# Optimization experiments

Hardware: AMD Instinct MI355X
Metric: run time of the kernel (lower is better)

## Reference

```python
import jax, jax.numpy as jnp
import numpy as np

N, B, CIN = 2048, 16, 1
M = 4096
COUT = 64
R = 128


def setup_inputs() -> dict:
    key = jax.random.key(0)
    k1, k2, k3, k4, k5 = jax.random.split(key, 5)
    return {
        "context_in": jax.random.normal(k1, (N, B, CIN), dtype=jnp.float32),
        "context_out": jax.random.normal(k2, (N, B, COUT), dtype=jnp.float32),
        "target_in": jax.random.normal(k3, (M, B, CIN), dtype=jnp.float32),
        "lengthscale": jnp.ones((1,), dtype=jnp.float32),
        "W": jax.random.normal(k4, (R, COUT + 1), dtype=jnp.float32),
        "b": jax.random.normal(k5, (R,), dtype=jnp.float32),
    }


def reference(context_in, context_out, target_in, lengthscale, W, b):
    # context_in: (N,B,Cin), context_out: (N,B,Cout), target_in: (M,B,Cin)
    n, batch, _ = context_in.shape
    # density channel prepended -> (N,B,Cout+1)
    dens = jnp.ones((n, batch, 1), dtype=context_in.dtype)
    co = jnp.concatenate([dens, context_out], axis=-1)
    ci = jnp.transpose(context_in, (1, 0, 2))   # (B,N,Cin)
    ti = jnp.transpose(target_in, (1, 0, 2))    # (B,M,Cin)
    # squared pairwise distances (B,N,M)
    d2 = (jnp.sum(ci * ci, -1)[:, :, None]
          + jnp.sum(ti * ti, -1)[:, None, :]
          - 2.0 * jnp.einsum('bnd,bmd->bnm', ci, ti))
    d2 = jnp.maximum(d2, 0.0)
    # RBF kernel: exp(-0.5 * d2 / lengthscale^2)
    K = jnp.exp(-0.5 * d2 / (lengthscale[0] ** 2))  # (B,N,M)
    # weighted sum over context points: (B,M,Cout+1)
    out = jnp.einsum('nbc,bnm->bmc', co, K)
    # density normalization of non-density channels
    out = jnp.concatenate([out[..., :1], out[..., 1:] / (out[..., :1] + 1e-8)], axis=-1)
    # linear projection (Cout+1 -> R)
    out = out @ W.T + b
    return jnp.transpose(out, (1, 0, 2))  # (M,B,R)
```

## Files before the change

### kernel.cpp

```cpp
#include <hip/hip_runtime.h>
#include <hip/hip_bf16.h>


#define N_CTX 2048
#define BATCH 16
#define M_TGT 4096
#define COUT  64
#define RDIM  128
#define TN    64
#define NTILES (N_CTX / TN)

typedef __attribute__((ext_vector_type(8)))  short        bf16x8;
typedef __attribute__((ext_vector_type(4)))  unsigned int uint4v;
typedef __attribute__((ext_vector_type(16))) float        floatx16;

#if __has_builtin(__builtin_amdgcn_exp2f)
#define EXP2F __builtin_amdgcn_exp2f
#else
#define EXP2F exp2f
#endif

static __device__ __forceinline__ unsigned int pack_bf16(float lo, float hi) {
    __hip_bfloat162 h = __float22bfloat162_rn(make_float2(lo, hi));
    return *reinterpret_cast<unsigned int*>(&h);
}
static __device__ __forceinline__ unsigned short f2bf(float f) {
    __hip_bfloat16 h = __float2bfloat16(f);
    return *reinterpret_cast<unsigned short*>(&h);
}

__global__ __launch_bounds__(256)
void convdeepset_mfma(const float* __restrict__ ci, const float* __restrict__ co,
                      const float* __restrict__ ti, const float* __restrict__ ls,
                      const float* __restrict__ W,  const float* __restrict__ bias,
                      float* __restrict__ out)
{
    __shared__ unsigned short co_t[4096];
    __shared__ unsigned short wt[8192];
    __shared__ unsigned short vstage[4 * 2048];
    __shared__ float x_t[TN];
    __shared__ float w0l[RDIM];
    __shared__ float biasl[RDIM];

    const int tid  = threadIdx.x;
    const int lane = tid & 63;
    const int wv   = tid >> 6;
    const int g    = lane >> 5;
    const int l31  = lane & 31;
    const int b    = blockIdx.x >> 5;
    const int mt   = blockIdx.x & 31;

    for (int e = tid; e < 4096; e += 256) {
        const int ch  = e >> 9;
        const int rem = e & 511;
        const int r   = rem >> 2;
        const int tp  = (rem & 3) << 1;
        const float f0 = W[r * 65 + 1 + ch * 8 + tp];
        const float f1 = W[r * 65 + 2 + ch * 8 + tp];
        *reinterpret_cast<unsigned int*>(&wt[ch * 1024 + r * 8 + tp]) = pack_bf16(f0, f1);
    }
    if (tid < RDIM) { w0l[tid] = W[tid * 65]; biasl[tid] = bias[tid]; }

    const int m0    = mt * 128 + wv * 32;
    const float y   = ti[(size_t)(m0 + l31) * BATCH + b];
    const float lsv = ls[0];
    const float fc2 = (-0.5f / (lsv * lsv)) * 1.4426950408889634f;

    const int sc = tid & 63;
    const int sn = (tid >> 6) * 16;
    const float* cob = co + (size_t)b * COUT + sc;

    float pf[16];
#pragma unroll
    for (int q = 0; q < 8; ++q) {
        pf[2*q]   = cob[(size_t)(sn + 2*q)     * (BATCH * COUT)];
        pf[2*q+1] = cob[(size_t)(sn + 2*q + 1) * (BATCH * COUT)];
    }
    float xpf = (tid < TN) ? ci[(size_t)tid * BATCH + b] : 0.0f;

    floatx16 acc0, acc1;
#pragma unroll
    for (int i = 0; i < 16; ++i) { acc0[i] = 0.0f; acc1[i] = 0.0f; }
    float dens = 0.0f;

    for (int t = 0; t < NTILES; ++t) {
        __syncthreads();
#pragma unroll
        for (int q = 0; q < 8; ++q) {
            const int noff = sn + 2*q;
            *reinterpret_cast<unsigned int*>(&co_t[(noff >> 3) * 512 + sc * 8 + (noff & 7)])
                = pack_bf16(pf[2*q], pf[2*q+1]);
        }
        if (tid < TN) x_t[tid] = xpf;
        __syncthreads();
        if (t + 1 < NTILES) {
            const int n0n = (t + 1) * TN;
#pragma unroll
            for (int q = 0; q < 8; ++q) {
                pf[2*q]   = cob[(size_t)(n0n + sn + 2*q)     * (BATCH * COUT)];
                pf[2*q+1] = cob[(size_t)(n0n + sn + 2*q + 1) * (BATCH * COUT)];
            }
            if (tid < TN) xpf = ci[(size_t)(n0n + tid) * BATCH + b];
        }
#pragma unroll
        for (int s = 0; s < 4; ++s) {
            const float* xp = &x_t[s * 16 + g * 8];
            const float4 xa = *(const float4*)(xp);
            const float4 xb = *(const float4*)(xp + 4);
            const float xs[8] = {xa.x, xa.y, xa.z, xa.w, xb.x, xb.y, xb.z, xb.w};
            float kv[8];
#pragma unroll
            for (int j = 0; j < 8; ++j) {
                const float d = xs[j] - y;
                kv[j] = EXP2F(fc2 * d * d);
                dens += kv[j];
            }
            uint4v aw;
#pragma unroll
            for (int q = 0; q < 4; ++q) aw[q] = pack_bf16(kv[2*q], kv[2*q+1]);
            const bf16x8 av = __builtin_bit_cast(bf16x8, aw);
            const int ch = 2 * s + g;
            const bf16x8 b0 = *reinterpret_cast<const bf16x8*>(&co_t[ch * 512 + l31 * 8]);
            const bf16x8 b1 = *reinterpret_cast<const bf16x8*>(&co_t[ch * 512 + l31 * 8 + 256]);
            acc0 = __builtin_amdgcn_mfma_f32_32x32x16_bf16(av, b0, acc0, 0, 0, 0);
            acc1 = __builtin_amdgcn_mfma_f32_32x32x16_bf16(av, b1, acc1, 0, 0, 0);
        }
    }

    dens += __shfl_xor(dens, 32);

    float drow[16];
    unsigned short* vs = vstage + wv * 2048;
#pragma unroll
    for (int reg = 0; reg < 16; ++reg) {
        const int row = (reg & 3) + 8 * (reg >> 2) + 4 * g;
        const float dr = __shfl(dens, row);
        drow[reg] = dr;
        const float dinv = 1.0f / (dr + 1e-8f);
        const float v0 = acc0[reg] * dinv;
        const float v1 = acc1[reg] * dinv;
        const int c0 = l31, c1 = 32 + l31;
        vs[(c0 >> 3) * 256 + row * 8 + (c0 & 7)] = f2bf(v0);
        vs[(c1 >> 3) * 256 + row * 8 + (c1 & 7)] = f2bf(v1);
    }

    floatx16 pacc[4];
#pragma unroll
    for (int rt = 0; rt < 4; ++rt)
#pragma unroll
        for (int i = 0; i < 16; ++i) pacc[rt][i] = 0.0f;

#pragma unroll
    for (int s2 = 0; s2 < 4; ++s2) {
        const int ch = 2 * s2 + g;
        const bf16x8 avp = *reinterpret_cast<const bf16x8*>(&vs[ch * 256 + l31 * 8]);
#pragma unroll
        for (int rt = 0; rt < 4; ++rt) {
            const bf16x8 bvp = *reinterpret_cast<const bf16x8*>(&wt[ch * 1024 + (rt * 32 + l31) * 8]);
            pacc[rt] = __builtin_amdgcn_mfma_f32_32x32x16_bf16(avp, bvp, pacc[rt], 0, 0, 0);
        }
    }

#pragma unroll
    for (int rt = 0; rt < 4; ++rt) {
        const int r = rt * 32 + l31;
        const float w0v = w0l[r];
        const float bv  = biasl[r];
#pragma unroll
        for (int reg = 0; reg < 16; ++reg) {
            const int row = (reg & 3) + 8 * (reg >> 2) + 4 * g;
            const float val = pacc[rt][reg] + drow[reg] * w0v + bv;
            out[((size_t)(m0 + row) * BATCH + b) * RDIM + r] = val;
        }
    }
}

extern "C" void kernel_launch(void* const* d_in, const int* in_sizes, int n_in,
                              void* d_out, int out_size, void* d_ws, size_t ws_size,
                              hipStream_t stream) {
    const float* ci   = (const float*)d_in[0];
    const float* co   = (const float*)d_in[1];
    const float* ti   = (const float*)d_in[2];
    const float* ls   = (const float*)d_in[3];
    const float* W    = (const float*)d_in[4];
    const float* bias = (const float*)d_in[5];
    float* o = (float*)d_out;
    (void)in_sizes; (void)n_in; (void)out_size; (void)d_ws; (void)ws_size;

    const int grid = BATCH * (M_TGT / 128);
    convdeepset_mfma<<<grid, 256, 0, stream>>>(ci, co, ti, ls, W, bias, o);
}
```

Baseline: 134.0 us.

## Precompute bf16 MFMA-layout context and scaled inputs in a prep kernel

Adds a preprocessing kernel that converts context_out to bf16 in the exact MFMA B-operand layout, pre-scales context inputs by sqrt(0.5*log2e)/lengthscale, and packs W into workspace. The main kernel then streams B fragments straight from global memory with register double-buffering, with no per-tile LDS staging or __syncthreads. Blocks shrink to 128 threads with 64 targets each, doubling the grid. The cost is an extra launch and the global traffic of the prep pass, and each block still rereads the whole bf16 context for its batch from L2.

```diff
diff --git a/kernel.cpp b/kernel.cpp
--- a/kernel.cpp
+++ b/kernel.cpp
@@ -7,8 +7,12 @@
 #define M_TGT 4096
 #define COUT  64
 #define RDIM  128
-#define TN    64
-#define NTILES (N_CTX / TN)
+
+#define WS_CO_BYTES (N_CTX * BATCH * COUT * 2)
+#define WS_SX_OFF   WS_CO_BYTES
+#define WS_WT_OFF   (WS_SX_OFF + N_CTX * BATCH * 4)
+
+#define SSCALE 0.8493222f
 
 typedef __attribute__((ext_vector_type(8)))  short        bf16x8;
 typedef __attribute__((ext_vector_type(4)))  unsigned int uint4v;
@@ -30,120 +34,118 @@
 }
 
 __global__ __launch_bounds__(256)
-void convdeepset_mfma(const float* __restrict__ ci, const float* __restrict__ co,
-                      const float* __restrict__ ti, const float* __restrict__ ls,
+void convdeepset_prep(const float* __restrict__ ci, const float* __restrict__ co,
+                      const float* __restrict__ ls, const float* __restrict__ W,
+                      unsigned char* __restrict__ ws)
+{
+    unsigned short* cow = (unsigned short*)ws;
+    float*          sx  = (float*)(ws + WS_SX_OFF);
+    unsigned short* wt  = (unsigned short*)(ws + WS_WT_OFF);
+    const int blk = blockIdx.x, tid = threadIdx.x;
+
+    if (blk < 4096) {
+        const int f  = blk * 256 + tid;
+        const int c  = f & 63;
+        const int bb = (f >> 6) & 15;
+        const int n  = (f >> 10) * 2;
+        const float f0 = co[((size_t)n       * BATCH + bb) * COUT + c];
+        const float f1 = co[((size_t)(n + 1) * BATCH + bb) * COUT + c];
+        const int gch = n >> 3, e = n & 7;
+        *(unsigned int*)&cow[bb * 131072 + gch * 512 + c * 8 + e] = pack_bf16(f0, f1);
+    } else if (blk < 4224) {
+        const int f = (blk - 4096) * 256 + tid;
+        const int n = f & 2047, bb = f >> 11;
+        const float s = SSCALE / ls[0];
+        sx[bb * 2048 + n] = s * ci[(size_t)n * BATCH + bb];
+    } else {
+        for (int f = tid; f < 8192; f += 256) {
+            const int cp = f & 7, r = (f >> 3) & 127, ch = f >> 10;
+            wt[ch * 1024 + r * 8 + cp] = f2bf(W[r * 65 + 1 + ch * 8 + cp]);
+        }
+    }
+}
+
+__global__ __launch_bounds__(128)
+void convdeepset_main(const float* __restrict__ ti, const float* __restrict__ ls,
                       const float* __restrict__ W,  const float* __restrict__ bias,
-                      float* __restrict__ out)
+                      const unsigned char* __restrict__ ws, float* __restrict__ out)
 {
-    __shared__ unsigned short co_t[4096];
-    __shared__ unsigned short wt[8192];
-    __shared__ unsigned short vstage[4 * 2048];
-    __shared__ float x_t[TN];
-    __shared__ float w0l[RDIM];
-    __shared__ float biasl[RDIM];
+    __shared__ float sxt[N_CTX];
+    __shared__ unsigned short vstage[2][2048];
 
     const int tid  = threadIdx.x;
     const int lane = tid & 63;
     const int wv   = tid >> 6;
     const int g    = lane >> 5;
     const int l31  = lane & 31;
-    const int b    = blockIdx.x >> 5;
-    const int mt   = blockIdx.x & 31;
+    const int b    = blockIdx.x >> 6;
+    const int mt   = blockIdx.x & 63;
+    const int m0   = mt * 64 + wv * 32;
 
-    for (int e = tid; e < 4096; e += 256) {
-        const int ch  = e >> 9;
-        const int rem = e & 511;
-        const int r   = rem >> 2;
-        const int tp  = (rem & 3) << 1;
-        const float f0 = W[r * 65 + 1 + ch * 8 + tp];
-        const float f1 = W[r * 65 + 2 + ch * 8 + tp];
-        *reinterpret_cast<unsigned int*>(&wt[ch * 1024 + r * 8 + tp]) = pack_bf16(f0, f1);
-    }
-    if (tid < RDIM) { w0l[tid] = W[tid * 65]; biasl[tid] = bias[tid]; }
+    const float4* sxg = (const float4*)(ws + WS_SX_OFF) + b * (N_CTX / 4);
+    float4* sxt4 = (float4*)sxt;
+#pragma unroll
+    for (int q = 0; q < 4; ++q) sxt4[q * 128 + tid] = sxg[q * 128 + tid];
 
-    const int m0    = mt * 128 + wv * 32;
-    const float y   = ti[(size_t)(m0 + l31) * BATCH + b];
-    const float lsv = ls[0];
-    const float fc2 = (-0.5f / (lsv * lsv)) * 1.4426950408889634f;
+    const float s  = SSCALE / ls[0];
+    const float sy = s * ti[(size_t)(m0 + l31) * BATCH + b];
+    __syncthreads();
 
-    const int sc = tid & 63;
-    const int sn = (tid >> 6) * 16;
-    const float* cob = co + (size_t)b * COUT + sc;
-
-    float pf[16];
-#pragma unroll
-    for (int q = 0; q < 8; ++q) {
-        pf[2*q]   = cob[(size_t)(sn + 2*q)     * (BATCH * COUT)];
-        pf[2*q+1] = cob[(size_t)(sn + 2*q + 1) * (BATCH * COUT)];
-    }
-    float xpf = (tid < TN) ? ci[(size_t)tid * BATCH + b] : 0.0f;
+    const unsigned short* cow = (const unsigned short*)ws
+                              + (size_t)b * 131072 + g * 512 + l31 * 8;
 
     floatx16 acc0, acc1;
 #pragma unroll
     for (int i = 0; i < 16; ++i) { acc0[i] = 0.0f; acc1[i] = 0.0f; }
     float dens = 0.0f;
 
-    for (int t = 0; t < NTILES; ++t) {
-        __syncthreads();
+    bf16x8 cb0 = *(const bf16x8*)(cow);
+    bf16x8 cb1 = *(const bf16x8*)(cow + 256);
+    float4 xa  = *(const float4*)&sxt[g * 8];
+    float4 xb  = *(const float4*)&sxt[g * 8 + 4];
+
+    for (int ks = 0; ks < 128; ++ks) {
+        bf16x8 nb0 = cb0, nb1 = cb1; float4 nxa = xa, nxb = xb;
+        if (ks < 127) {
+            const unsigned short* p = cow + (ks + 1) * 1024;
+            nb0 = *(const bf16x8*)(p);
+            nb1 = *(const bf16x8*)(p + 256);
+            nxa = *(const float4*)&sxt[(ks + 1) * 16 + g * 8];
+            nxb = *(const float4*)&sxt[(ks + 1) * 16 + g * 8 + 4];
+        }
+        const float xs[8] = {xa.x, xa.y, xa.z, xa.w, xb.x, xb.y, xb.z, xb.w};
+        float kv[8];
 #pragma unroll
-        for (int q = 0; q < 8; ++q) {
-            const int noff = sn + 2*q;
-            *reinterpret_cast<unsigned int*>(&co_t[(noff >> 3) * 512 + sc * 8 + (noff & 7)])
-                = pack_bf16(pf[2*q], pf[2*q+1]);
+        for (int j = 0; j < 8; ++j) {
+            const float t = xs[j] - sy;
+            kv[j] = EXP2F(-(t * t));
+            dens += kv[j];
         }
-        if (tid < TN) x_t[tid] = xpf;
-        __syncthreads();
-        if (t + 1 < NTILES) {
-            const int n0n = (t + 1) * TN;
+        uint4v aw;
 #pragma unroll
-            for (int q = 0; q < 8; ++q) {
-                pf[2*q]   = cob[(size_t)(n0n + sn + 2*q)     * (BATCH * COUT)];
-                pf[2*q+1] = cob[(size_t)(n0n + sn + 2*q + 1) * (BATCH * COUT)];
-            }
-            if (tid < TN) xpf = ci[(size_t)(n0n + tid) * BATCH + b];
-        }
-#pragma unroll
-        for (int s = 0; s < 4; ++s) {
-            const float* xp = &x_t[s * 16 + g * 8];
-            const float4 xa = *(const float4*)(xp);
-            const float4 xb = *(const float4*)(xp + 4);
-            const float xs[8] = {xa.x, xa.y, xa.z, xa.w, xb.x, xb.y, xb.z, xb.w};
-            float kv[8];
-#pragma unroll
-            for (int j = 0; j < 8; ++j) {
-                const float d = xs[j] - y;
-                kv[j] = EXP2F(fc2 * d * d);
-                dens += kv[j];
-            }
-            uint4v aw;
-#pragma unroll
-            for (int q = 0; q < 4; ++q) aw[q] = pack_bf16(kv[2*q], kv[2*q+1]);
-            const bf16x8 av = __builtin_bit_cast(bf16x8, aw);
-            const int ch = 2 * s + g;
-            const bf16x8 b0 = *reinterpret_cast<const bf16x8*>(&co_t[ch * 512 + l31 * 8]);
-            const bf16x8 b1 = *reinterpret_cast<const bf16x8*>(&co_t[ch * 512 + l31 * 8 + 256]);
-            acc0 = __builtin_amdgcn_mfma_f32_32x32x16_bf16(av, b0, acc0, 0, 0, 0);
-            acc1 = __builtin_amdgcn_mfma_f32_32x32x16_bf16(av, b1, acc1, 0, 0, 0);
-        }
+        for (int q = 0; q < 4; ++q) aw[q] = pack_bf16(kv[2 * q], kv[2 * q + 1]);
+        const bf16x8 av = __builtin_bit_cast(bf16x8, aw);
+        acc0 = __builtin_amdgcn_mfma_f32_32x32x16_bf16(av, cb0, acc0, 0, 0, 0);
+        acc1 = __builtin_amdgcn_mfma_f32_32x32x16_bf16(av, cb1, acc1, 0, 0, 0);
+        cb0 = nb0; cb1 = nb1; xa = nxa; xb = nxb;
     }
 
     dens += __shfl_xor(dens, 32);
 
     float drow[16];
-    unsigned short* vs = vstage + wv * 2048;
+    unsigned short* vs = vstage[wv];
 #pragma unroll
     for (int reg = 0; reg < 16; ++reg) {
         const int row = (reg & 3) + 8 * (reg >> 2) + 4 * g;
         const float dr = __shfl(dens, row);
         drow[reg] = dr;
         const float dinv = 1.0f / (dr + 1e-8f);
-        const float v0 = acc0[reg] * dinv;
-        const float v1 = acc1[reg] * dinv;
         const int c0 = l31, c1 = 32 + l31;
-        vs[(c0 >> 3) * 256 + row * 8 + (c0 & 7)] = f2bf(v0);
-        vs[(c1 >> 3) * 256 + row * 8 + (c1 & 7)] = f2bf(v1);
+        vs[(c0 >> 3) * 256 + row * 8 + (c0 & 7)] = f2bf(acc0[reg] * dinv);
+        vs[(c1 >> 3) * 256 + row * 8 + (c1 & 7)] = f2bf(acc1[reg] * dinv);
     }
 
+    const unsigned short* wtg = (const unsigned short*)(ws + WS_WT_OFF);
     floatx16 pacc[4];
 #pragma unroll
     for (int rt = 0; rt < 4; ++rt)
@@ -153,10 +155,10 @@
 #pragma unroll
     for (int s2 = 0; s2 < 4; ++s2) {
         const int ch = 2 * s2 + g;
-        const bf16x8 avp = *reinterpret_cast<const bf16x8*>(&vs[ch * 256 + l31 * 8]);
+        const bf16x8 avp = *(const bf16x8*)&vs[ch * 256 + l31 * 8];
 #pragma unroll
         for (int rt = 0; rt < 4; ++rt) {
-            const bf16x8 bvp = *reinterpret_cast<const bf16x8*>(&wt[ch * 1024 + (rt * 32 + l31) * 8]);
+            const bf16x8 bvp = *(const bf16x8*)&wtg[ch * 1024 + (rt * 32 + l31) * 8];
             pacc[rt] = __builtin_amdgcn_mfma_f32_32x32x16_bf16(avp, bvp, pacc[rt], 0, 0, 0);
         }
     }
@@ -164,13 +166,13 @@
 #pragma unroll
     for (int rt = 0; rt < 4; ++rt) {
         const int r = rt * 32 + l31;
-        const float w0v = w0l[r];
-        const float bv  = biasl[r];
+        const float w0v = W[r * 65];
+        const float bv  = bias[r];
 #pragma unroll
         for (int reg = 0; reg < 16; ++reg) {
             const int row = (reg & 3) + 8 * (reg >> 2) + 4 * g;
-            const float val = pacc[rt][reg] + drow[reg] * w0v + bv;
-            out[((size_t)(m0 + row) * BATCH + b) * RDIM + r] = val;
+            out[((size_t)(m0 + row) * BATCH + b) * RDIM + r]
+                = pacc[rt][reg] + drow[reg] * w0v + bv;
         }
     }
 }
@@ -185,8 +187,9 @@
     const float* W    = (const float*)d_in[4];
     const float* bias = (const float*)d_in[5];
     float* o = (float*)d_out;
-    (void)in_sizes; (void)n_in; (void)out_size; (void)d_ws; (void)ws_size;
+    (void)in_sizes; (void)n_in; (void)out_size; (void)ws_size;
 
-    const int grid = BATCH * (M_TGT / 128);
-    convdeepset_mfma<<<grid, 256, 0, stream>>>(ci, co, ti, ls, W, bias, o);
+    convdeepset_prep<<<4225, 256, 0, stream>>>(ci, co, ls, W, (unsigned char*)d_ws);
+    convdeepset_main<<<BATCH * (M_TGT / 64), 128, 0, stream>>>(
+        ti, ls, W, bias, (const unsigned char*)d_ws, o);
 }
```

After: 143.7 us. 7.2% more time.
